# Kernel tuning notes

Measured on AMD Instinct MI355X. Metric: run time of the kernel, lower is better.

## Reference

```python
import jax, jax.numpy as jnp
import numpy as np

D = 1024
NUM_HEADS = 16
HEAD_SIZE = D // NUM_HEADS  # scaling factor only; no actual head split in original

def setup_inputs() -> dict:
    key = jax.random.key(0)
    ks = jax.random.split(key, 9)
    B, S = 4, 2048
    inp = {
        'incorporacao': jax.random.normal(ks[0], (B, S, D), dtype=jnp.float32),
        'Wq': jax.random.normal(ks[1], (D, D), dtype=jnp.float32) * (1.0 / np.sqrt(D)),
        'bq': jnp.zeros((D,), dtype=jnp.float32),
        'Wk': jax.random.normal(ks[2], (D, D), dtype=jnp.float32) * (1.0 / np.sqrt(D)),
        'bk': jnp.zeros((D,), dtype=jnp.float32),
        'Wv': jax.random.normal(ks[3], (D, D), dtype=jnp.float32) * (1.0 / np.sqrt(D)),
        'bv': jnp.zeros((D,), dtype=jnp.float32),
        'Wo': jax.random.normal(ks[4], (D, D), dtype=jnp.float32) * (1.0 / np.sqrt(D)),
        'bo': jnp.zeros((D,), dtype=jnp.float32),
    }
    return inp

def reference(incorporacao, Wq, bq, Wk, bk, Wv, bv, Wo, bo):
    # Faithful to original: NO head split; attention over full embedding dim,
    # scaled by sqrt(head_size) = sqrt(D / num_cabecas).
    q = jnp.einsum('bsd,df->bsf', incorporacao, Wq) + bq  # [B,S,D]
    k = jnp.einsum('bsd,df->bsf', incorporacao, Wk) + bk
    v = jnp.einsum('bsd,df->bsf', incorporacao, Wv) + bv
    scores = jnp.einsum('bsd,btd->bst', q, k) / jnp.sqrt(jnp.float32(HEAD_SIZE))  # [B,S,S]
    attn = jax.nn.softmax(scores, axis=-1)
    ctx = jnp.einsum('bst,btd->bsd', attn, v)  # [B,S,D]
    out = jnp.einsum('bsd,df->bsf', ctx, Wo) + bo
    return out
```

## Files before the change

### kernel.cpp

```cpp
#include <hip/hip_runtime.h>
#include <cstdint>
#include <cstddef>

typedef unsigned short u16;
typedef __attribute__((ext_vector_type(8))) short short8;
typedef __attribute__((ext_vector_type(4))) float f32x4;

#define BB 4
#define SS 2048
#define DD 1024

__device__ __forceinline__ u16 f2bf(float f) {
  union { float f; unsigned u; } x; x.f = f;
  unsigned r = x.u + 0x7FFFu + ((x.u >> 16) & 1u);
  return (u16)(r >> 16);
}

__device__ __forceinline__ void gld_lds16(const void* g, void* l) {
  __builtin_amdgcn_global_load_lds(
      (const __attribute__((address_space(1))) void*)g,
      (__attribute__((address_space(3))) void*)l, 16, 0, 0);
}

__device__ __forceinline__ void store_out(float* p, float v) { *p = v; }
__device__ __forceinline__ void store_out(u16* p, float v) { *p = f2bf(v); }

template<typename OutT, int BM, int MODE, bool HAS_BIAS>
__global__ __launch_bounds__(512, 2) void gemm8p(
    const u16* __restrict__ A, size_t sA, int ldaB,
    const u16* __restrict__ B, size_t sB, int ldbB,
    OutT* __restrict__ C, size_t sC, int ldc,
    const float* __restrict__ bias, float scale, int K,
    u16* __restrict__ out2, u16* __restrict__ out3)
{
  constexpr int MF    = BM / 32;
  constexpr int ASLOT = BM * 32;
  constexpr int ASETS = BM / 128;
  constexpr int L     = ASETS + 2;
  __shared__ u16 sm[4 * ASLOT + 4 * 8192];

  const int gx = gridDim.x, gy = gridDim.y;
  const int nwg = gx * gy * gridDim.z;
  const int flat = blockIdx.x + gx * (blockIdx.y + gy * blockIdx.z);
  const int swz = (flat & 7) * (nwg >> 3) + (flat >> 3);
  const int bz  = swz / (gx * gy);
  const int rem = swz - bz * (gx * gy);
  const int by  = rem / gx;
  const int bx  = rem - by * gx;
  const int blockM = by * BM, blockN = bx * 256;

  const char* Abase = (const char*)(A + (size_t)bz * sA);
  const char* Bbase = (const char*)(B + (size_t)bz * sB);

  const int tid  = threadIdx.x;
  const int wave = tid >> 6, lane = tid & 63;
  const int wrow = (wave >> 2) * (BM / 2);
  const int wcol = (wave & 3) * 64;

  const int sr  = tid >> 2;
  const int scb = ((tid & 3) * 16) ^ (((sr >> 1) & 3) << 4);
  const char* gA0 = Abase + (size_t)(blockM + sr) * ldaB + scb;
  const char* gA1 = (ASETS == 2) ? Abase + (size_t)(blockM + sr + 128) * ldaB + scb
                                 : nullptr;
  const char* gB0 = Bbase + (size_t)(blockN + sr)       * ldbB + scb;
  const char* gB1 = Bbase + (size_t)(blockN + sr + 128) * ldbB + scb;
  const int ldsw = wave * 512;

  auto STAGE = [&](int r) {
    gld_lds16(gA0, sm + r * ASLOT + ldsw);
    if constexpr (ASETS == 2) gld_lds16(gA1, sm + r * ASLOT + 4096 + ldsw);
    gld_lds16(gB0, sm + 4 * ASLOT + r * 8192 + ldsw);
    gld_lds16(gB1, sm + 4 * ASLOT + r * 8192 + 4096 + ldsw);
    gA0 += 64; gB0 += 64; gB1 += 64;
    if constexpr (ASETS == 2) gA1 += 64;
  };

  const int r16 = lane & 15, q8 = (lane >> 4) * 8;
  int offA[MF], offB[4];
#pragma unroll
  for (int mi = 0; mi < MF; ++mi) {
    const int row = wrow + mi * 16 + r16;
    offA[mi] = row * 32 + (q8 ^ (((row >> 1) & 3) << 3));
  }
#pragma unroll
  for (int nj = 0; nj < 4; ++nj) {
    const int row = wcol + nj * 16 + r16;
    offB[nj] = row * 32 + (q8 ^ (((row >> 1) & 3) << 3));
  }

  f32x4 acc[MF][4] = {};
  const int NP = K >> 5;

  STAGE(0); STAGE(1); STAGE(2);
  asm volatile("s_waitcnt vmcnt(%0)" :: "i"(2 * L) : "memory");
  __builtin_amdgcn_s_barrier();
  __builtin_amdgcn_sched_barrier(0);

  for (int p = 0; p < NP; ++p) {
    const int ring = p & 3;
    const u16* As = sm + ring * ASLOT;
    const u16* Bs = sm + 4 * ASLOT + ring * 8192;

    short8 bfv[4], af[MF];
#pragma unroll
    for (int nj = 0; nj < 4; ++nj) bfv[nj] = *(const short8*)(Bs + offB[nj]);
#pragma unroll
    for (int mi = 0; mi < MF; ++mi) af[mi] = *(const short8*)(As + offA[mi]);

    if (p < NP - 2)       asm volatile("s_waitcnt vmcnt(%0)" :: "i"(L) : "memory");
    else if (p == NP - 2) asm volatile("s_waitcnt vmcnt(0)" ::: "memory");
    __builtin_amdgcn_s_barrier();
    __builtin_amdgcn_sched_barrier(0);

    if (p + 3 < NP) STAGE((p + 3) & 3);

    __builtin_amdgcn_s_setprio(1);
#pragma unroll
    for (int mi = 0; mi < MF; ++mi)
#pragma unroll
      for (int nj = 0; nj < 4; ++nj)
        acc[mi][nj] = __builtin_amdgcn_mfma_f32_16x16x32_bf16(
            af[mi], bfv[nj], acc[mi][nj], 0, 0, 0);
    __builtin_amdgcn_s_setprio(0);
    __builtin_amdgcn_sched_barrier(0);
  }

  const int cr = lane & 15, rr0 = (lane >> 4) * 4;
  OutT* Cb = C + (size_t)bz * sC;
#pragma unroll
  for (int nj = 0; nj < 4; ++nj) {
    const int colg = blockN + wcol + nj * 16 + cr;
    const float bval = HAS_BIAS ? bias[colg] : 0.0f;
#pragma unroll
    for (int mi = 0; mi < MF; ++mi) {
      f32x4 v = acc[mi][nj];
      const int rowg = blockM + wrow + mi * 16 + rr0;
      if constexpr (MODE == 0) {
#pragma unroll
        for (int i = 0; i < 4; ++i)
          store_out(&Cb[(size_t)(rowg + i) * ldc + colg], v[i] * scale + bval);
      } else {
        if (colg < 2048) {
          u16* dst = (colg < 1024) ? (u16*)Cb : out2;
          const int c2 = colg & 1023;
#pragma unroll
          for (int i = 0; i < 4; ++i)
            dst[(size_t)(rowg + i) * 1024 + c2] = f2bf(v[i] + bval);
        } else {
          const int d  = colg - 2048;
          const int b  = rowg >> 11;
          const int t0 = rowg & 2047;
          u16 h0 = f2bf(v[0] + bval), h1 = f2bf(v[1] + bval);
          u16 h2 = f2bf(v[2] + bval), h3 = f2bf(v[3] + bval);
          uint2 u;
          u.x = (unsigned)h0 | ((unsigned)h1 << 16);
          u.y = (unsigned)h2 | ((unsigned)h3 << 16);
          *(uint2*)&out3[((size_t)b * 1024 + d) * 2048 + t0] = u;
        }
      }
    }
  }
}

__global__ __launch_bounds__(256) void cvt_f32_bf16(
    const float* __restrict__ in, u16* __restrict__ out, int n4)
{
  int i = blockIdx.x * 256 + threadIdx.x;
  if (i >= n4) return;
  float4 v = ((const float4*)in)[i];
  uint2 u;
  u.x = (unsigned)f2bf(v.x) | ((unsigned)f2bf(v.y) << 16);
  u.y = (unsigned)f2bf(v.z) | ((unsigned)f2bf(v.w) << 16);
  ((uint2*)out)[i] = u;
}

__global__ __launch_bounds__(256) void transpose_cvt(
    const float* __restrict__ W, u16* __restrict__ Wt)
{
  __shared__ u16 tile[32][33];
  const int tx = threadIdx.x;
  const int ty = threadIdx.y;
  const int bx = blockIdx.x * 32;
  const int by = blockIdx.y * 32;
#pragma unroll
  for (int j = 0; j < 4; ++j) {
    int d = by + ty * 4 + j;
    tile[ty * 4 + j][tx] = f2bf(W[(size_t)d * DD + bx + tx]);
  }
  __syncthreads();
#pragma unroll
  for (int j = 0; j < 4; ++j) {
    int f = bx + ty * 4 + j;
    Wt[(size_t)f * DD + by + tx] = tile[tx][ty * 4 + j];
  }
}

__global__ __launch_bounds__(256) void concat_bias(
    const float* __restrict__ bq, const float* __restrict__ bk,
    const float* __restrict__ bv, float* __restrict__ out)
{
  int i = blockIdx.x * 256 + threadIdx.x;
  const float* src = (i < 1024) ? bq : ((i < 2048) ? bk : bv);
  out[i] = src[i & 1023];
}

__global__ __launch_bounds__(256) void softmax_inplace(float* __restrict__ S)
{
  const int tid = threadIdx.x;
  float* rp = S + (size_t)blockIdx.x * SS;

  float4 v0 = ((const float4*)rp)[tid];
  float4 v1 = ((const float4*)rp)[tid + 256];

  float m = fmaxf(fmaxf(fmaxf(v0.x, v0.y), fmaxf(v0.z, v0.w)),
                  fmaxf(fmaxf(v1.x, v1.y), fmaxf(v1.z, v1.w)));
#pragma unroll
  for (int off = 32; off; off >>= 1) m = fmaxf(m, __shfl_xor(m, off));

  __shared__ float smax[4];
  __shared__ float ssum[4];
  const int wave = tid >> 6, lane = tid & 63;
  if (lane == 0) smax[wave] = m;
  __syncthreads();
  m = fmaxf(fmaxf(smax[0], smax[1]), fmaxf(smax[2], smax[3]));

  float e[8];
  e[0] = __expf(v0.x - m); e[1] = __expf(v0.y - m);
  e[2] = __expf(v0.z - m); e[3] = __expf(v0.w - m);
  e[4] = __expf(v1.x - m); e[5] = __expf(v1.y - m);
  e[6] = __expf(v1.z - m); e[7] = __expf(v1.w - m);
  float s = e[0] + e[1] + e[2] + e[3] + e[4] + e[5] + e[6] + e[7];
#pragma unroll
  for (int off = 32; off; off >>= 1) s += __shfl_xor(s, off);
  if (lane == 0) ssum[wave] = s;
  __syncthreads();
  float inv = 1.0f / (ssum[0] + ssum[1] + ssum[2] + ssum[3]);

  uint2 u0, u1;
  u0.x = (unsigned)f2bf(e[0] * inv) | ((unsigned)f2bf(e[1] * inv) << 16);
  u0.y = (unsigned)f2bf(e[2] * inv) | ((unsigned)f2bf(e[3] * inv) << 16);
  u1.x = (unsigned)f2bf(e[4] * inv) | ((unsigned)f2bf(e[5] * inv) << 16);
  u1.y = (unsigned)f2bf(e[6] * inv) | ((unsigned)f2bf(e[7] * inv) << 16);
  ((uint2*)rp)[tid]       = u0;
  ((uint2*)rp)[tid + 256] = u1;
}

extern "C" void kernel_launch(void* const* d_in, const int* in_sizes, int n_in,
                              void* d_out, int out_size, void* d_ws, size_t ws_size,
                              hipStream_t stream) {
  (void)in_sizes; (void)n_in; (void)out_size; (void)ws_size;
  const float* X  = (const float*)d_in[0];
  const float* Wq = (const float*)d_in[1];
  const float* bq = (const float*)d_in[2];
  const float* Wk = (const float*)d_in[3];
  const float* bk = (const float*)d_in[4];
  const float* Wv = (const float*)d_in[5];
  const float* bv = (const float*)d_in[6];
  const float* Wo = (const float*)d_in[7];
  const float* bo = (const float*)d_in[8];

  char* ws = (char*)d_ws;
  const size_t MBy = 1ull << 20;
  u16*   Xbf   = (u16*)(ws + 0);
  u16*   WtAll = (u16*)(ws + 16 * MBy);
  u16*   Wto   = (u16*)(ws + 22 * MBy);
  u16*   Qb    = (u16*)(ws + 24 * MBy);
  u16*   Kb    = (u16*)(ws + 40 * MBy);
  u16*   Vt    = (u16*)(ws + 56 * MBy);
  float* Sf    = (float*)(ws + 72 * MBy);
  float* bqkv  = (float*)(ws + 72 * MBy);
  u16*   Ctx   = (u16*)(ws + 136 * MBy);

  cvt_f32_bf16<<<dim3((BB * SS * DD / 4) / 256), 256, 0, stream>>>(X, Xbf, BB * SS * DD / 4);
  dim3 tb(32, 8);
  transpose_cvt<<<dim3(32, 32), tb, 0, stream>>>(Wq, WtAll);
  transpose_cvt<<<dim3(32, 32), tb, 0, stream>>>(Wk, WtAll + 1024 * 1024);
  transpose_cvt<<<dim3(32, 32), tb, 0, stream>>>(Wv, WtAll + 2 * 1024 * 1024);
  transpose_cvt<<<dim3(32, 32), tb, 0, stream>>>(Wo, Wto);
  concat_bias<<<dim3(12), 256, 0, stream>>>(bq, bk, bv, bqkv);

  gemm8p<u16, 256, 1, true><<<dim3(12, 32, 1), 512, 0, stream>>>(
      Xbf, 0, DD * 2, WtAll, 0, DD * 2,
      Qb, 0, 0, bqkv, 1.0f, DD, Kb, Vt);

  gemm8p<float, 256, 0, false><<<dim3(8, 8, BB), 512, 0, stream>>>(
      Qb, (size_t)SS * DD, DD * 2, Kb, (size_t)SS * DD, DD * 2,
      Sf, (size_t)SS * SS, SS, nullptr, 0.125f, DD, nullptr, nullptr);

  softmax_inplace<<<dim3(BB * SS), 256, 0, stream>>>(Sf);

  gemm8p<u16, 128, 0, false><<<dim3(4, 16, BB), 512, 0, stream>>>(
      (const u16*)Sf, (size_t)SS * 2 * SS, 2 * SS * 2,
      Vt, (size_t)DD * SS, SS * 2,
      Ctx, (size_t)SS * DD, DD, nullptr, 1.0f, SS, nullptr, nullptr);

  gemm8p<float, 128, 0, true><<<dim3(4, 64, 1), 512, 0, stream>>>(
      Ctx, 0, DD * 2, Wto, 0, DD * 2,
      (float*)d_out, 0, DD, bo, 1.0f, DD, nullptr, nullptr);
}
```

Before: 216.6 us.

## Fix GEMM tile at 128x256 with register double-buffered LDS reads

Removes the BM=256 variant so every GEMM uses 128x256 tiles. The QKV and QK^T launches get twice as many M-blocks to compensate. The main loop is unrolled by two, with ping-pong register fragments so LDS reads for the next k-step overlap the current MFMAs. For the transposed V output, the MFMA operands are swapped so the accumulator is already transposed, and stores go straight to Vt. This trades per-block data reuse for more blocks and better latency hiding, and the new V stores write one element at a time.

```diff
diff --git a/kernel.cpp b/kernel.cpp
--- a/kernel.cpp
+++ b/kernel.cpp
@@ -25,7 +25,7 @@
 __device__ __forceinline__ void store_out(float* p, float v) { *p = v; }
 __device__ __forceinline__ void store_out(u16* p, float v) { *p = f2bf(v); }
 
-template<typename OutT, int BM, int MODE, bool HAS_BIAS>
+template<typename OutT, int MODE, bool HAS_BIAS>
 __global__ __launch_bounds__(512, 2) void gemm8p(
     const u16* __restrict__ A, size_t sA, int ldaB,
     const u16* __restrict__ B, size_t sB, int ldbB,
@@ -33,10 +33,8 @@
     const float* __restrict__ bias, float scale, int K,
     u16* __restrict__ out2, u16* __restrict__ out3)
 {
-  constexpr int MF    = BM / 32;
-  constexpr int ASLOT = BM * 32;
-  constexpr int ASETS = BM / 128;
-  constexpr int L     = ASETS + 2;
+  constexpr int ASLOT = 128 * 32;
+  constexpr int L     = 3;
   __shared__ u16 sm[4 * ASLOT + 4 * 8192];
 
   const int gx = gridDim.x, gy = gridDim.y;
@@ -47,38 +45,34 @@
   const int rem = swz - bz * (gx * gy);
   const int by  = rem / gx;
   const int bx  = rem - by * gx;
-  const int blockM = by * BM, blockN = bx * 256;
+  const int blockM = by * 128, blockN = bx * 256;
 
   const char* Abase = (const char*)(A + (size_t)bz * sA);
   const char* Bbase = (const char*)(B + (size_t)bz * sB);
 
   const int tid  = threadIdx.x;
   const int wave = tid >> 6, lane = tid & 63;
-  const int wrow = (wave >> 2) * (BM / 2);
+  const int wrow = (wave >> 2) * 64;
   const int wcol = (wave & 3) * 64;
 
   const int sr  = tid >> 2;
   const int scb = ((tid & 3) * 16) ^ (((sr >> 1) & 3) << 4);
-  const char* gA0 = Abase + (size_t)(blockM + sr) * ldaB + scb;
-  const char* gA1 = (ASETS == 2) ? Abase + (size_t)(blockM + sr + 128) * ldaB + scb
-                                 : nullptr;
+  const char* gA0 = Abase + (size_t)(blockM + sr)       * ldaB + scb;
   const char* gB0 = Bbase + (size_t)(blockN + sr)       * ldbB + scb;
   const char* gB1 = Bbase + (size_t)(blockN + sr + 128) * ldbB + scb;
   const int ldsw = wave * 512;
 
   auto STAGE = [&](int r) {
     gld_lds16(gA0, sm + r * ASLOT + ldsw);
-    if constexpr (ASETS == 2) gld_lds16(gA1, sm + r * ASLOT + 4096 + ldsw);
     gld_lds16(gB0, sm + 4 * ASLOT + r * 8192 + ldsw);
     gld_lds16(gB1, sm + 4 * ASLOT + r * 8192 + 4096 + ldsw);
     gA0 += 64; gB0 += 64; gB1 += 64;
-    if constexpr (ASETS == 2) gA1 += 64;
   };
 
   const int r16 = lane & 15, q8 = (lane >> 4) * 8;
-  int offA[MF], offB[4];
-#pragma unroll
-  for (int mi = 0; mi < MF; ++mi) {
+  int offA[4], offB[4];
+#pragma unroll
+  for (int mi = 0; mi < 4; ++mi) {
     const int row = wrow + mi * 16 + r16;
     offA[mi] = row * 32 + (q8 ^ (((row >> 1) & 3) << 3));
   }
@@ -88,74 +82,102 @@
     offB[nj] = row * 32 + (q8 ^ (((row >> 1) & 3) << 3));
   }
 
-  f32x4 acc[MF][4] = {};
+  auto READ = [&](short8* af, short8* bv, int ring) {
+    const u16* As = sm + ring * ASLOT;
+    const u16* Bs = sm + 4 * ASLOT + ring * 8192;
+#pragma unroll
+    for (int nj = 0; nj < 4; ++nj) bv[nj] = *(const short8*)(Bs + offB[nj]);
+#pragma unroll
+    for (int mi = 0; mi < 4; ++mi) af[mi] = *(const short8*)(As + offA[mi]);
+  };
+
+  f32x4 acc[4][4] = {};
+  const bool vblk = (MODE == 1) && (blockN >= 2048);
+
+  auto MMA = [&](short8* af, short8* bv) {
+    __builtin_amdgcn_s_setprio(1);
+    if (vblk) {
+#pragma unroll
+      for (int mi = 0; mi < 4; ++mi)
+#pragma unroll
+        for (int nj = 0; nj < 4; ++nj)
+          acc[mi][nj] = __builtin_amdgcn_mfma_f32_16x16x32_bf16(
+              bv[nj], af[mi], acc[mi][nj], 0, 0, 0);
+    } else {
+#pragma unroll
+      for (int mi = 0; mi < 4; ++mi)
+#pragma unroll
+        for (int nj = 0; nj < 4; ++nj)
+          acc[mi][nj] = __builtin_amdgcn_mfma_f32_16x16x32_bf16(
+              af[mi], bv[nj], acc[mi][nj], 0, 0, 0);
+    }
+    __builtin_amdgcn_s_setprio(0);
+  };
+
+  short8 a0[4], b0[4], a1[4], b1[4];
   const int NP = K >> 5;
 
   STAGE(0); STAGE(1); STAGE(2);
   asm volatile("s_waitcnt vmcnt(%0)" :: "i"(2 * L) : "memory");
   __builtin_amdgcn_s_barrier();
   __builtin_amdgcn_sched_barrier(0);
-
-  for (int p = 0; p < NP; ++p) {
-    const int ring = p & 3;
-    const u16* As = sm + ring * ASLOT;
-    const u16* Bs = sm + 4 * ASLOT + ring * 8192;
-
-    short8 bfv[4], af[MF];
-#pragma unroll
-    for (int nj = 0; nj < 4; ++nj) bfv[nj] = *(const short8*)(Bs + offB[nj]);
-#pragma unroll
-    for (int mi = 0; mi < MF; ++mi) af[mi] = *(const short8*)(As + offA[mi]);
-
-    if (p < NP - 2)       asm volatile("s_waitcnt vmcnt(%0)" :: "i"(L) : "memory");
-    else if (p == NP - 2) asm volatile("s_waitcnt vmcnt(0)" ::: "memory");
+  READ(a0, b0, 0);
+
+  for (int p = 0; p < NP; p += 2) {
+    if (p + 2 < NP) asm volatile("s_waitcnt vmcnt(%0)" :: "i"(L) : "memory");
+    else            asm volatile("s_waitcnt vmcnt(0)" ::: "memory");
     __builtin_amdgcn_s_barrier();
     __builtin_amdgcn_sched_barrier(0);
-
     if (p + 3 < NP) STAGE((p + 3) & 3);
-
-    __builtin_amdgcn_s_setprio(1);
-#pragma unroll
-    for (int mi = 0; mi < MF; ++mi)
-#pragma unroll
-      for (int nj = 0; nj < 4; ++nj)
-        acc[mi][nj] = __builtin_amdgcn_mfma_f32_16x16x32_bf16(
-            af[mi], bfv[nj], acc[mi][nj], 0, 0, 0);
-    __builtin_amdgcn_s_setprio(0);
+    if (p + 1 < NP) READ(a1, b1, (p + 1) & 3);
+    MMA(a0, b0);
+
+    if (p + 3 < NP) asm volatile("s_waitcnt vmcnt(%0)" :: "i"(L) : "memory");
+    else            asm volatile("s_waitcnt vmcnt(0)" ::: "memory");
+    __builtin_amdgcn_s_barrier();
     __builtin_amdgcn_sched_barrier(0);
+    if (p + 4 < NP) STAGE((p + 4) & 3);
+    if (p + 2 < NP) READ(a0, b0, (p + 2) & 3);
+    MMA(a1, b1);
   }
 
   const int cr = lane & 15, rr0 = (lane >> 4) * 4;
   OutT* Cb = C + (size_t)bz * sC;
-#pragma unroll
-  for (int nj = 0; nj < 4; ++nj) {
-    const int colg = blockN + wcol + nj * 16 + cr;
-    const float bval = HAS_BIAS ? bias[colg] : 0.0f;
-#pragma unroll
-    for (int mi = 0; mi < MF; ++mi) {
-      f32x4 v = acc[mi][nj];
-      const int rowg = blockM + wrow + mi * 16 + rr0;
-      if constexpr (MODE == 0) {
-#pragma unroll
-        for (int i = 0; i < 4; ++i)
-          store_out(&Cb[(size_t)(rowg + i) * ldc + colg], v[i] * scale + bval);
-      } else {
-        if (colg < 2048) {
+  if (vblk) {
+#pragma unroll
+    for (int nj = 0; nj < 4; ++nj) {
+#pragma unroll
+      for (int mi = 0; mi < 4; ++mi) {
+        f32x4 v = acc[mi][nj];
+        const int tg = blockM + wrow + mi * 16 + cr;
+        const int b  = tg >> 11, t0 = tg & 2047;
+        const int d0 = blockN - 2048 + wcol + nj * 16 + rr0;
+#pragma unroll
+        for (int i = 0; i < 4; ++i) {
+          const float bval = HAS_BIAS ? bias[2048 + d0 + i] : 0.0f;
+          out3[((size_t)b * 1024 + d0 + i) * 2048 + t0] = f2bf(v[i] + bval);
+        }
+      }
+    }
+  } else {
+#pragma unroll
+    for (int nj = 0; nj < 4; ++nj) {
+      const int colg = blockN + wcol + nj * 16 + cr;
+      const float bval = HAS_BIAS ? bias[colg] : 0.0f;
+#pragma unroll
+      for (int mi = 0; mi < 4; ++mi) {
+        f32x4 v = acc[mi][nj];
+        const int rowg = blockM + wrow + mi * 16 + rr0;
+        if constexpr (MODE == 0) {
+#pragma unroll
+          for (int i = 0; i < 4; ++i)
+            store_out(&Cb[(size_t)(rowg + i) * ldc + colg], v[i] * scale + bval);
+        } else {
           u16* dst = (colg < 1024) ? (u16*)Cb : out2;
           const int c2 = colg & 1023;
 #pragma unroll
           for (int i = 0; i < 4; ++i)
             dst[(size_t)(rowg + i) * 1024 + c2] = f2bf(v[i] + bval);
-        } else {
-          const int d  = colg - 2048;
-          const int b  = rowg >> 11;
-          const int t0 = rowg & 2047;
-          u16 h0 = f2bf(v[0] + bval), h1 = f2bf(v[1] + bval);
-          u16 h2 = f2bf(v[2] + bval), h3 = f2bf(v[3] + bval);
-          uint2 u;
-          u.x = (unsigned)h0 | ((unsigned)h1 << 16);
-          u.y = (unsigned)h2 | ((unsigned)h3 << 16);
-          *(uint2*)&out3[((size_t)b * 1024 + d) * 2048 + t0] = u;
         }
       }
     }
@@ -279,22 +301,22 @@
   transpose_cvt<<<dim3(32, 32), tb, 0, stream>>>(Wo, Wto);
   concat_bias<<<dim3(12), 256, 0, stream>>>(bq, bk, bv, bqkv);
 
-  gemm8p<u16, 256, 1, true><<<dim3(12, 32, 1), 512, 0, stream>>>(
+  gemm8p<u16, 1, true><<<dim3(12, 64, 1), 512, 0, stream>>>(
       Xbf, 0, DD * 2, WtAll, 0, DD * 2,
       Qb, 0, 0, bqkv, 1.0f, DD, Kb, Vt);
 
-  gemm8p<float, 256, 0, false><<<dim3(8, 8, BB), 512, 0, stream>>>(
+  gemm8p<float, 0, false><<<dim3(8, 16, BB), 512, 0, stream>>>(
       Qb, (size_t)SS * DD, DD * 2, Kb, (size_t)SS * DD, DD * 2,
       Sf, (size_t)SS * SS, SS, nullptr, 0.125f, DD, nullptr, nullptr);
 
   softmax_inplace<<<dim3(BB * SS), 256, 0, stream>>>(Sf);
 
-  gemm8p<u16, 128, 0, false><<<dim3(4, 16, BB), 512, 0, stream>>>(
+  gemm8p<u16, 0, false><<<dim3(4, 16, BB), 512, 0, stream>>>(
       (const u16*)Sf, (size_t)SS * 2 * SS, 2 * SS * 2,
       Vt, (size_t)DD * SS, SS * 2,
       Ctx, (size_t)SS * DD, DD, nullptr, 1.0f, SS, nullptr, nullptr);
 
-  gemm8p<float, 128, 0, true><<<dim3(4, 64, 1), 512, 0, stream>>>(
+  gemm8p<float, 0, true><<<dim3(4, 64, 1), 512, 0, stream>>>(
       Ctx, 0, DD * 2, Wto, 0, DD * 2,
       (float*)d_out, 0, DD, bo, 1.0f, DD, nullptr, nullptr);
 }
```

Measured after the change: 219.1 us. No clear change (+1.2%).
